# Performance work log

Measured on AMD Instinct MI355X. Metric: run time of the kernel, lower is better.

Reference implementation:

```python
import jax, jax.numpy as jnp
import numpy as np

B, T, D = 16, 2048, 256
QK = 64


def setup_inputs() -> dict:
    key = jax.random.key(0)
    ks = jax.random.split(key, 9)
    x = jax.random.normal(ks[0], (B, T, D), dtype=jnp.float32)
    sl = jax.random.uniform(ks[1], (B, T), dtype=jnp.float32)
    mask = jax.random.randint(ks[2], (B, T), 0, 2, dtype=jnp.int32)
    s = 1.0 / np.sqrt(D).astype(np.float32)
    Wq = jax.random.normal(ks[3], (QK, D), dtype=jnp.float32) * s
    bq = jnp.zeros((QK,), dtype=jnp.float32)
    Wk = jax.random.normal(ks[4], (QK, D), dtype=jnp.float32) * s
    bk = jnp.zeros((QK,), dtype=jnp.float32)
    Wv = jax.random.normal(ks[5], (D, D), dtype=jnp.float32) * s
    bv = jnp.zeros((D,), dtype=jnp.float32)
    return {"x": x, "sl": sl, "mask": mask, "Wq": Wq, "bq": bq,
            "Wk": Wk, "bk": bk, "Wv": Wv, "bv": bv}


def reference(x, sl, mask, Wq, bq, Wk, bk, Wv, bv):
    # x: [B,T,D], sl: [B,T] soft labels, mask: [B,T] valid positions
    sl = jnp.clip(sl, 0.0, 1.0)
    q = jnp.einsum('btd,ed->bte', x, Wq) + bq          # [B,T,QK]
    k = jnp.einsum('btd,ed->bte', x, Wk) + bk          # [B,T,QK]
    v = jnp.einsum('btd,ed->bte', x, Wv) + bv          # [B,T,D]
    scale = jnp.float32(1.0 / np.sqrt(QK))
    score = jnp.einsum('bte,bse->bts', q, k) * scale   # [B,T,T]
    # emotion scaling by (1 + sl_j^2) per key position j
    score = score * (1.0 + sl[:, None, :] ** 2)
    score = jnp.where(mask[:, None, :] == 0, jnp.float32(-1e9), score)
    prob = jax.nn.softmax(score, axis=-1)              # [B,T,T]
    out = jnp.einsum('bts,bsd->btd', prob, v)          # [B,T,D]
    return out.mean(axis=1)                            # [B,D]
```

## Files before the change

### kernel.cpp

```cpp
#include <hip/hip_runtime.h>
#include <hip/hip_bf16.h>
#include <stdint.h>

#define B_ 16
#define T_ 2048
#define D_ 256
#define QK_ 64
#define LOG2E 1.44269504088896340736f

typedef _Float16 f16;
typedef _Float16 f16x2 __attribute__((ext_vector_type(2)));
typedef __fp16 fp16x2 __attribute__((ext_vector_type(2)));
typedef _Float16 f16x8 __attribute__((ext_vector_type(8)));
typedef float f32x16 __attribute__((ext_vector_type(16)));

__device__ __forceinline__ void gload_lds16(const void* g, void* l) {
    __builtin_amdgcn_global_load_lds(
        (const __attribute__((address_space(1))) uint32_t*)g,
        (__attribute__((address_space(3))) uint32_t*)l, 16, 0, 0);
}

__device__ __forceinline__ float fexp2(float x) {
#if __has_builtin(__builtin_amdgcn_exp2f)
    return __builtin_amdgcn_exp2f(x);
#else
    return exp2f(x);
#endif
}
__device__ __forceinline__ float flog2(float x) {
#if __has_builtin(__builtin_amdgcn_logf)
    return __builtin_amdgcn_logf(x);
#else
    return log2f(x);
#endif
}
__device__ __forceinline__ f16x2 cvt2(float a, float b) {
#if __has_builtin(__builtin_amdgcn_cvt_pkrtz)
    fp16x2 r = __builtin_amdgcn_cvt_pkrtz(a, b);
    return __builtin_bit_cast(f16x2, r);
#else
    f16x2 r; r[0] = (f16)a; r[1] = (f16)b; return r;
#endif
}
__device__ __forceinline__ f16x8 cvt8(const float* p) {
    union { f16x2 h2[4]; f16x8 h8; } u;
    const float4 a0 = *(const float4*)p;
    const float4 a1 = *(const float4*)(p + 4);
    u.h2[0] = cvt2(a0.x, a0.y); u.h2[1] = cvt2(a0.z, a0.w);
    u.h2[2] = cvt2(a1.x, a1.y); u.h2[3] = cvt2(a1.z, a1.w);
    return u.h8;
}

__global__ __launch_bounds__(256) void proj_mfma(
    const float* __restrict__ x, const float* __restrict__ sl,
    const float* __restrict__ Wq, const float* __restrict__ Wk,
    const float* __restrict__ bq, const float* __restrict__ bk,
    f16* __restrict__ qh, f16* __restrict__ k2h,
    f16* __restrict__ qf, f16* __restrict__ kf)
{
    __shared__ __align__(16) f16 xs[32 * D_];
    __shared__ float ksc[32];
    const int b = blockIdx.y, tile = blockIdx.x, t0 = tile * 32;
    const int tid = threadIdx.x;
    const int wv = tid >> 6, l = tid & 63, lo = l & 31, hi = l >> 5;

    #pragma unroll
    for (int i = 0; i < 4; ++i) {
        const int f = i * 256 + tid;
        const int r = f >> 5, j = f & 31;
        const f16x8 h = cvt8(x + (size_t)(b * T_ + t0 + r) * D_ + j * 8);
        *(f16x8*)(xs + r * D_ + ((j ^ r) << 3)) = h;
    }
    if (tid < 32) {
        float s = sl[(size_t)b * T_ + t0 + tid];
        s = fminf(fmaxf(s, 0.f), 1.f);
        ksc[tid] = 0.125f * (1.f + s * s) * LOG2E;
    }
    __syncthreads();

    const int c0 = wv * 32;
    const int e = c0 + lo;
    const float* wrow = ((e < 64) ? (Wq + (size_t)e * D_)
                                  : (Wk + (size_t)(e - 64) * D_)) + hi * 8;

    f32x16 acc;
    #pragma unroll
    for (int i = 0; i < 16; ++i) acc[i] = 0.f;

    #pragma unroll
    for (int ks = 0; ks < 16; ++ks) {
        const f16x8 a  = *(const f16x8*)(xs + lo * D_ + ((((ks << 1) + hi) ^ lo) << 3));
        const f16x8 bf = cvt8(wrow + ks * 16);
        acc = __builtin_amdgcn_mfma_f32_32x32x16_f16(a, bf, acc, 0, 0, 0);
    }

    const float bias = (e < 64) ? bq[e] : bk[e - 64];
    __syncthreads();
    f16* hout = xs;
    #pragma unroll
    for (int i = 0; i < 16; ++i) {
        const int row = (i & 3) + 8 * (i >> 2) + 4 * hi;
        float v = acc[i] + bias;
        if (e >= 64) v *= ksc[row];
        hout[row * 128 + e] = (f16)v;
    }
    __syncthreads();
    #pragma unroll
    for (int i = 0; i < 2; ++i) {
        const int f = i * 256 + tid;
        const int rr = f >> 4, j = f & 15;
        const f16x8 v = *(const f16x8*)(hout + rr * 128 + j * 8);
        if (j < 8) *(f16x8*)(qh  + (size_t)(b * T_ + t0 + rr) * QK_ + j * 8) = v;
        else       *(f16x8*)(k2h + (size_t)(b * T_ + t0 + rr) * QK_ + (j - 8) * 8) = v;
    }
    {
        const int kc2 = tid >> 6, hi2 = (tid >> 5) & 1, lo2 = tid & 31;
        const f16* srcq = hout + lo2 * 128 + kc2 * 16 + hi2 * 8;
        const size_t tb = ((size_t)b * 64 + tile) * 2048 + tid * 8;
        *(f16x8*)(qf + tb) = *(const f16x8*)srcq;
        *(f16x8*)(kf + tb) = *(const f16x8*)(srcq + 64);
    }
}

__global__ __launch_bounds__(256) void z_part(
    const f16* __restrict__ qf, const f16* __restrict__ k2h,
    const int* __restrict__ mask, float* __restrict__ zpart)
{
    __shared__ __align__(16) f16 kt[128 * QK_];
    const int b = blockIdx.y;
    const int tIdx = blockIdx.x & 15, t0 = tIdx * 128;
    const int ck = blockIdx.x >> 4,  sbase = ck * 128;
    const int tid = threadIdx.x;
    const int wv = tid >> 6, l = tid & 63, lo = l & 31, hi = l >> 5;

    {
        const char* src = (const char*)(k2h + (size_t)(b * T_ + sbase) * QK_);
        #pragma unroll
        for (int i = 0; i < 4; ++i) {
            const int o = wv * 4096 + i * 1024 + l * 16;
            const int r = o >> 7, jc = (o >> 4) & 7;
            gload_lds16(src + r * 128 + ((jc ^ (r & 7)) << 4),
                        (char*)kt + wv * 4096 + i * 1024);
        }
    }

    const f16* abase = qf + ((size_t)b * 64 + tIdx * 4 + wv) * 2048 + l * 8;
    f16x8 a[4];
    #pragma unroll
    for (int kc = 0; kc < 4; ++kc) a[kc] = *(const f16x8*)(abase + kc * 512);

    float zp[16];
    #pragma unroll
    for (int i = 0; i < 16; ++i) zp[i] = 0.f;

    __syncthreads();

    #pragma unroll
    for (int cg = 0; cg < 4; ++cg) {
        const int srow = cg * 32 + lo;
        const float mb = mask[b * T_ + sbase + srow] ? 0.f : -1e9f;
        f32x16 c;
        #pragma unroll
        for (int i = 0; i < 16; ++i) c[i] = mb;
        #pragma unroll
        for (int kc = 0; kc < 4; ++kc) {
            const int jcc = (kc * 2 + hi) ^ (srow & 7);
            const f16x8 bf = *(const f16x8*)((const char*)kt + srow * 128 + (jcc << 4));
            c = __builtin_amdgcn_mfma_f32_32x32x16_f16(a[kc], bf, c, 0, 0, 0);
        }
        #pragma unroll
        for (int i = 0; i < 16; ++i) zp[i] += fexp2(c[i]);
    }

    __syncthreads();
    float* red = (float*)kt;
    #pragma unroll
    for (int i = 0; i < 16; ++i) {
        const int row = wv * 32 + (i & 3) + 8 * (i >> 2) + 4 * hi;
        const int col = (lo & 3) | ((((lo >> 2) ^ row) & 7) << 2);
        red[row * 32 + col] = zp[i];
    }
    __syncthreads();
    if (tid < 128) {
        float s = 0.f;
        #pragma unroll
        for (int c = 0; c < 8; ++c) {
            const float4 v = *(const float4*)(red + tid * 32 + (((c ^ tid) & 7) << 2));
            s += v.x + v.y + v.z + v.w;
        }
        zpart[(size_t)(b * 16 + ck) * T_ + t0 + tid] = s;
    }
}

__global__ __launch_bounds__(256) void w_part(
    const f16* __restrict__ kf, const f16* __restrict__ qh,
    const float* __restrict__ zpart, float* __restrict__ wpart)
{
    __shared__ __align__(16) f16 qt[128 * QK_];
    __shared__ float lz_s[128];
    const int b = blockIdx.y;
    const int sIdx = blockIdx.x & 15, s0b = sIdx * 128;
    const int tc = blockIdx.x >> 4,  tbase = tc * 128;
    const int tid = threadIdx.x;
    const int wv = tid >> 6, l = tid & 63, lo = l & 31, hi = l >> 5;

    {
        const char* src = (const char*)(qh + (size_t)(b * T_ + tbase) * QK_);
        #pragma unroll
        for (int i = 0; i < 4; ++i) {
            const int o = wv * 4096 + i * 1024 + l * 16;
            const int r = o >> 7, jc = (o >> 4) & 7;
            gload_lds16(src + r * 128 + ((jc ^ (r & 7)) << 4),
                        (char*)qt + wv * 4096 + i * 1024);
        }
    }
    if (tid < 128) {
        const float* zb = zpart + (size_t)(b * 16) * T_ + tbase + tid;
        float z = 0.f;
        #pragma unroll
        for (int ckk = 0; ckk < 16; ++ckk) z += zb[(size_t)ckk * T_];
        lz_s[tid] = -flog2(z);
    }

    const f16* abase = kf + ((size_t)b * 64 + sIdx * 4 + wv) * 2048 + l * 8;
    f16x8 a[4];
    #pragma unroll
    for (int kc = 0; kc < 4; ++kc) a[kc] = *(const f16x8*)(abase + kc * 512);

    float wp[16];
    #pragma unroll
    for (int i = 0; i < 16; ++i) wp[i] = 0.f;

    __syncthreads();

    #pragma unroll
    for (int cg = 0; cg < 4; ++cg) {
        const int trow = cg * 32 + lo;
        const float bias = lz_s[trow];
        f32x16 c;
        #pragma unroll
        for (int i = 0; i < 16; ++i) c[i] = bias;
        #pragma unroll
        for (int kc = 0; kc < 4; ++kc) {
            const int jcc = (kc * 2 + hi) ^ (trow & 7);
            const f16x8 bf = *(const f16x8*)((const char*)qt + trow * 128 + (jcc << 4));
            c = __builtin_amdgcn_mfma_f32_32x32x16_f16(a[kc], bf, c, 0, 0, 0);
        }
        #pragma unroll
        for (int i = 0; i < 16; ++i) wp[i] += fexp2(c[i]);
    }

    __syncthreads();
    float* red = (float*)qt;
    #pragma unroll
    for (int i = 0; i < 16; ++i) {
        const int row = wv * 32 + (i & 3) + 8 * (i >> 2) + 4 * hi;
        const int col = (lo & 3) | ((((lo >> 2) ^ row) & 7) << 2);
        red[row * 32 + col] = wp[i];
    }
    __syncthreads();
    if (tid < 128) {
        float s = 0.f;
        #pragma unroll
        for (int c = 0; c < 8; ++c) {
            const float4 v = *(const float4*)(red + tid * 32 + (((c ^ tid) & 7) << 2));
            s += v.x + v.y + v.z + v.w;
        }
        wpart[(size_t)(b * 16 + tc) * T_ + s0b + tid] = s;
    }
}

__global__ __launch_bounds__(256) void y_fused(
    const float* __restrict__ x, const float* __restrict__ wpart,
    const int* __restrict__ mask, float* __restrict__ ypart,
    float* __restrict__ swp)
{
    __shared__ float wloc[32];
    const int b  = blockIdx.y;
    const int ch = blockIdx.x;
    const int tid = threadIdx.x;

    if (tid < 32) {
        const int s = ch * 32 + tid;
        const float* wb = wpart + (size_t)(b * 16) * T_ + s;
        float v = 0.f;
        #pragma unroll
        for (int ckk = 0; ckk < 16; ++ckk) v += wb[(size_t)ckk * T_];
        v *= mask[b * T_ + s] ? (1.f / (float)T_) : 0.f;
        wloc[tid] = v;
        float sv = v;
        #pragma unroll
        for (int off = 1; off <= 16; off <<= 1) sv += __shfl_xor(sv, off);
        if (tid == 0) swp[b * 64 + ch] = sv;
    }
    __syncthreads();

    const int d = tid;
    const float* xb = x + ((size_t)b * T_ + ch * 32) * D_;
    float acc = 0.f;
    #pragma unroll 8
    for (int s = 0; s < 32; ++s) acc += wloc[s] * xb[(size_t)s * D_ + d];
    ypart[((size_t)b * 64 + ch) * D_ + d] = acc;
}

__global__ __launch_bounds__(256) void outkernel(
    const float* __restrict__ ypart, const float* __restrict__ swp,
    const float* __restrict__ Wv, const float* __restrict__ bv,
    float* __restrict__ out)
{
    __shared__ __align__(16) float ys[D_];
    __shared__ float sw0;
    const int b   = blockIdx.x;
    const int tid = threadIdx.x;

    float yv = 0.f;
    #pragma unroll
    for (int ch = 0; ch < 64; ++ch) yv += ypart[((size_t)b * 64 + ch) * D_ + tid];
    ys[tid] = yv;

    float s = (tid < 64) ? swp[b * 64 + tid] : 0.f;
    #pragma unroll
    for (int off = 1; off <= 32; off <<= 1) s += __shfl_xor(s, off);
    if (tid == 0) sw0 = s;
    __syncthreads();

    const float sw = sw0;
    const float4* wv4 = (const float4*)(Wv + (size_t)tid * D_);
    const float4* ys4 = (const float4*)ys;
    float o = 0.f;
    for (int i = 0; i < D_ / 4; ++i) {
        const float4 a = wv4[i];
        const float4 y = ys4[i];
        o += a.x * y.x + a.y * y.y + a.z * y.z + a.w * y.w;
    }
    out[(size_t)b * D_ + tid] = o + bv[tid] * sw;
}

extern "C" void kernel_launch(void* const* d_in, const int* in_sizes, int n_in,
                              void* d_out, int out_size, void* d_ws, size_t ws_size,
                              hipStream_t stream)
{
    const float* x    = (const float*)d_in[0];
    const float* sl   = (const float*)d_in[1];
    const int*   mask = (const int*)d_in[2];
    const float* Wq   = (const float*)d_in[3];
    const float* bq   = (const float*)d_in[4];
    const float* Wk   = (const float*)d_in[5];
    const float* bk   = (const float*)d_in[6];
    const float* Wv   = (const float*)d_in[7];
    const float* bv   = (const float*)d_in[8];
    float* out = (float*)d_out;

    f16*   qh    = (f16*)d_ws;
    f16*   k2h   = qh  + (size_t)B_ * T_ * QK_;
    f16*   qf    = k2h + (size_t)B_ * T_ * QK_;
    f16*   kf    = qf  + (size_t)B_ * T_ * QK_;
    float* zpart = (float*)(kf + (size_t)B_ * T_ * QK_);
    float* wpart = zpart + (size_t)B_ * 16 * T_;
    float* swp   = wpart + (size_t)B_ * 16 * T_;
    float* yp    = swp + B_ * 64;

    proj_mfma<<<dim3(T_ / 32, B_), 256, 0, stream>>>(x, sl, Wq, Wk, bq, bk, qh, k2h, qf, kf);
    z_part   <<<dim3(256, B_), 256, 0, stream>>>(qf, k2h, mask, zpart);
    w_part   <<<dim3(256, B_), 256, 0, stream>>>(kf, qh, zpart, wpart);
    y_fused  <<<dim3(64, B_), 256, 0, stream>>>(x, wpart, mask, yp, swp);
    outkernel<<<dim3(B_), 256, 0, stream>>>(yp, swp, Wv, bv, out);
}
```

Measured before the change: 82.60 us.

## Read fragment-layout K/Q directly from global and halve key-chunk split

The score kernels stop staging row-major K/Q tiles into LDS via global_load_lds and instead read MFMA-fragment-ordered q/k buffers directly from global memory into registers. This removes the qh/k2h outputs from the projection kernel. Each block now covers 256 key or query positions instead of 128, so there are half as many partial chunks to reduce and half as many blocks. In exchange, operand loads go through global/L2 without LDS reuse across waves, and grids are smaller, which lowers parallelism.

```diff
diff --git a/kernel.cpp b/kernel.cpp
--- a/kernel.cpp
+++ b/kernel.cpp
@@ -1,5 +1,4 @@
 #include <hip/hip_runtime.h>
-#include <hip/hip_bf16.h>
 #include <stdint.h>
 
 #define B_ 16
@@ -7,18 +6,13 @@
 #define D_ 256
 #define QK_ 64
 #define LOG2E 1.44269504088896340736f
+#define NCH 8
 
 typedef _Float16 f16;
 typedef _Float16 f16x2 __attribute__((ext_vector_type(2)));
 typedef __fp16 fp16x2 __attribute__((ext_vector_type(2)));
 typedef _Float16 f16x8 __attribute__((ext_vector_type(8)));
 typedef float f32x16 __attribute__((ext_vector_type(16)));
-
-__device__ __forceinline__ void gload_lds16(const void* g, void* l) {
-    __builtin_amdgcn_global_load_lds(
-        (const __attribute__((address_space(1))) uint32_t*)g,
-        (__attribute__((address_space(3))) uint32_t*)l, 16, 0, 0);
-}
 
 __device__ __forceinline__ float fexp2(float x) {
 #if __has_builtin(__builtin_amdgcn_exp2f)
@@ -51,18 +45,18 @@
     return u.h8;
 }
 
-__global__ __launch_bounds__(256) void proj_mfma(
+
+__global__ __launch_bounds__(256, 4) void kP(
     const float* __restrict__ x, const float* __restrict__ sl,
-    const float* __restrict__ Wq, const float* __restrict__ Wk,
-    const float* __restrict__ bq, const float* __restrict__ bk,
-    f16* __restrict__ qh, f16* __restrict__ k2h,
+    const float* __restrict__ Wq, const float* __restrict__ bq,
+    const float* __restrict__ Wk, const float* __restrict__ bk,
     f16* __restrict__ qf, f16* __restrict__ kf)
 {
     __shared__ __align__(16) f16 xs[32 * D_];
     __shared__ float ksc[32];
+    const int tid = threadIdx.x;
+    const int wv = tid >> 6, l = tid & 63, lo = l & 31, hi = l >> 5;
     const int b = blockIdx.y, tile = blockIdx.x, t0 = tile * 32;
-    const int tid = threadIdx.x;
-    const int wv = tid >> 6, l = tid & 63, lo = l & 31, hi = l >> 5;
 
     #pragma unroll
     for (int i = 0; i < 4; ++i) {
@@ -78,22 +72,18 @@
     }
     __syncthreads();
 
-    const int c0 = wv * 32;
-    const int e = c0 + lo;
+    const int e = wv * 32 + lo;
     const float* wrow = ((e < 64) ? (Wq + (size_t)e * D_)
                                   : (Wk + (size_t)(e - 64) * D_)) + hi * 8;
-
     f32x16 acc;
     #pragma unroll
     for (int i = 0; i < 16; ++i) acc[i] = 0.f;
-
     #pragma unroll
     for (int ks = 0; ks < 16; ++ks) {
         const f16x8 a  = *(const f16x8*)(xs + lo * D_ + ((((ks << 1) + hi) ^ lo) << 3));
         const f16x8 bf = cvt8(wrow + ks * 16);
         acc = __builtin_amdgcn_mfma_f32_32x32x16_f16(a, bf, acc, 0, 0, 0);
     }
-
     const float bias = (e < 64) ? bq[e] : bk[e - 64];
     __syncthreads();
     f16* hout = xs;
@@ -105,44 +95,22 @@
         hout[row * 128 + e] = (f16)v;
     }
     __syncthreads();
-    #pragma unroll
-    for (int i = 0; i < 2; ++i) {
-        const int f = i * 256 + tid;
-        const int rr = f >> 4, j = f & 15;
-        const f16x8 v = *(const f16x8*)(hout + rr * 128 + j * 8);
-        if (j < 8) *(f16x8*)(qh  + (size_t)(b * T_ + t0 + rr) * QK_ + j * 8) = v;
-        else       *(f16x8*)(k2h + (size_t)(b * T_ + t0 + rr) * QK_ + (j - 8) * 8) = v;
-    }
-    {
-        const int kc2 = tid >> 6, hi2 = (tid >> 5) & 1, lo2 = tid & 31;
-        const f16* srcq = hout + lo2 * 128 + kc2 * 16 + hi2 * 8;
-        const size_t tb = ((size_t)b * 64 + tile) * 2048 + tid * 8;
-        *(f16x8*)(qf + tb) = *(const f16x8*)srcq;
-        *(f16x8*)(kf + tb) = *(const f16x8*)(srcq + 64);
-    }
-}
-
-__global__ __launch_bounds__(256) void z_part(
-    const f16* __restrict__ qf, const f16* __restrict__ k2h,
+    const int kc2 = tid >> 6, hi2 = (tid >> 5) & 1, lo2 = tid & 31;
+    const f16* srcq = hout + lo2 * 128 + kc2 * 16 + hi2 * 8;
+    const size_t tb = ((size_t)b * 64 + tile) * 2048 + tid * 8;
+    *(f16x8*)(qf + tb) = *(const f16x8*)srcq;
+    *(f16x8*)(kf + tb) = *(const f16x8*)(srcq + 64);
+}
+
+__global__ __launch_bounds__(256, 4) void kZ(
+    const f16* __restrict__ qf, const f16* __restrict__ kf,
     const int* __restrict__ mask, float* __restrict__ zpart)
 {
-    __shared__ __align__(16) f16 kt[128 * QK_];
+    __shared__ __align__(16) float red[128 * 32];
+    const int tid = threadIdx.x;
+    const int wv = tid >> 6, l = tid & 63, lo = l & 31, hi = l >> 5;
     const int b = blockIdx.y;
-    const int tIdx = blockIdx.x & 15, t0 = tIdx * 128;
-    const int ck = blockIdx.x >> 4,  sbase = ck * 128;
-    const int tid = threadIdx.x;
-    const int wv = tid >> 6, l = tid & 63, lo = l & 31, hi = l >> 5;
-
-    {
-        const char* src = (const char*)(k2h + (size_t)(b * T_ + sbase) * QK_);
-        #pragma unroll
-        for (int i = 0; i < 4; ++i) {
-            const int o = wv * 4096 + i * 1024 + l * 16;
-            const int r = o >> 7, jc = (o >> 4) & 7;
-            gload_lds16(src + r * 128 + ((jc ^ (r & 7)) << 4),
-                        (char*)kt + wv * 4096 + i * 1024);
-        }
-    }
+    const int tIdx = blockIdx.x >> 3, ckg = blockIdx.x & 7;
 
     const f16* abase = qf + ((size_t)b * 64 + tIdx * 4 + wv) * 2048 + l * 8;
     f16x8 a[4];
@@ -153,27 +121,22 @@
     #pragma unroll
     for (int i = 0; i < 16; ++i) zp[i] = 0.f;
 
-    __syncthreads();
-
-    #pragma unroll
-    for (int cg = 0; cg < 4; ++cg) {
-        const int srow = cg * 32 + lo;
-        const float mb = mask[b * T_ + sbase + srow] ? 0.f : -1e9f;
+    #pragma unroll
+    for (int g = 0; g < 8; ++g) {
+        const int stile = ckg * 8 + g;
+        const float mb = mask[b * T_ + stile * 32 + lo] ? 0.f : -1e9f;
+        const f16* bbase = kf + ((size_t)b * 64 + stile) * 2048 + l * 8;
         f32x16 c;
         #pragma unroll
         for (int i = 0; i < 16; ++i) c[i] = mb;
         #pragma unroll
         for (int kc = 0; kc < 4; ++kc) {
-            const int jcc = (kc * 2 + hi) ^ (srow & 7);
-            const f16x8 bf = *(const f16x8*)((const char*)kt + srow * 128 + (jcc << 4));
+            const f16x8 bf = *(const f16x8*)(bbase + kc * 512);
             c = __builtin_amdgcn_mfma_f32_32x32x16_f16(a[kc], bf, c, 0, 0, 0);
         }
         #pragma unroll
         for (int i = 0; i < 16; ++i) zp[i] += fexp2(c[i]);
     }
-
-    __syncthreads();
-    float* red = (float*)kt;
     #pragma unroll
     for (int i = 0; i < 16; ++i) {
         const int row = wv * 32 + (i & 3) + 8 * (i >> 2) + 4 * hi;
@@ -188,40 +151,28 @@
             const float4 v = *(const float4*)(red + tid * 32 + (((c ^ tid) & 7) << 2));
             s += v.x + v.y + v.z + v.w;
         }
-        zpart[(size_t)(b * 16 + ck) * T_ + t0 + tid] = s;
-    }
-}
-
-__global__ __launch_bounds__(256) void w_part(
-    const f16* __restrict__ kf, const f16* __restrict__ qh,
+        zpart[(size_t)(b * NCH + ckg) * T_ + tIdx * 128 + tid] = s;
+    }
+}
+
+__global__ __launch_bounds__(256, 4) void kW(
+    const f16* __restrict__ qf, const f16* __restrict__ kf,
     const float* __restrict__ zpart, float* __restrict__ wpart)
 {
-    __shared__ __align__(16) f16 qt[128 * QK_];
-    __shared__ float lz_s[128];
+    __shared__ __align__(16) float red[128 * 32];
+    __shared__ float lz_s[256];
+    const int tid = threadIdx.x;
+    const int wv = tid >> 6, l = tid & 63, lo = l & 31, hi = l >> 5;
     const int b = blockIdx.y;
-    const int sIdx = blockIdx.x & 15, s0b = sIdx * 128;
-    const int tc = blockIdx.x >> 4,  tbase = tc * 128;
-    const int tid = threadIdx.x;
-    const int wv = tid >> 6, l = tid & 63, lo = l & 31, hi = l >> 5;
+    const int sIdx = blockIdx.x >> 3, tcg = blockIdx.x & 7;
 
     {
-        const char* src = (const char*)(qh + (size_t)(b * T_ + tbase) * QK_);
-        #pragma unroll
-        for (int i = 0; i < 4; ++i) {
-            const int o = wv * 4096 + i * 1024 + l * 16;
-            const int r = o >> 7, jc = (o >> 4) & 7;
-            gload_lds16(src + r * 128 + ((jc ^ (r & 7)) << 4),
-                        (char*)qt + wv * 4096 + i * 1024);
-        }
-    }
-    if (tid < 128) {
-        const float* zb = zpart + (size_t)(b * 16) * T_ + tbase + tid;
+        const float* zb = zpart + (size_t)(b * NCH) * T_ + tcg * 256 + tid;
         float z = 0.f;
         #pragma unroll
-        for (int ckk = 0; ckk < 16; ++ckk) z += zb[(size_t)ckk * T_];
+        for (int ck = 0; ck < NCH; ++ck) z += zb[(size_t)ck * T_];
         lz_s[tid] = -flog2(z);
     }
-
     const f16* abase = kf + ((size_t)b * 64 + sIdx * 4 + wv) * 2048 + l * 8;
     f16x8 a[4];
     #pragma unroll
@@ -230,28 +181,24 @@
     float wp[16];
     #pragma unroll
     for (int i = 0; i < 16; ++i) wp[i] = 0.f;
-
-    __syncthreads();
-
-    #pragma unroll
-    for (int cg = 0; cg < 4; ++cg) {
-        const int trow = cg * 32 + lo;
-        const float bias = lz_s[trow];
+    __syncthreads();
+
+    #pragma unroll
+    for (int g = 0; g < 8; ++g) {
+        const int qtile = tcg * 8 + g;
+        const float bias = lz_s[g * 32 + lo];
+        const f16* bbase = qf + ((size_t)b * 64 + qtile) * 2048 + l * 8;
         f32x16 c;
         #pragma unroll
         for (int i = 0; i < 16; ++i) c[i] = bias;
         #pragma unroll
         for (int kc = 0; kc < 4; ++kc) {
-            const int jcc = (kc * 2 + hi) ^ (trow & 7);
-            const f16x8 bf = *(const f16x8*)((const char*)qt + trow * 128 + (jcc << 4));
+            const f16x8 bf = *(const f16x8*)(bbase + kc * 512);
             c = __builtin_amdgcn_mfma_f32_32x32x16_f16(a[kc], bf, c, 0, 0, 0);
         }
         #pragma unroll
         for (int i = 0; i < 16; ++i) wp[i] += fexp2(c[i]);
     }
-
-    __syncthreads();
-    float* red = (float*)qt;
     #pragma unroll
     for (int i = 0; i < 16; ++i) {
         const int row = wv * 32 + (i & 3) + 8 * (i >> 2) + 4 * hi;
@@ -266,11 +213,11 @@
             const float4 v = *(const float4*)(red + tid * 32 + (((c ^ tid) & 7) << 2));
             s += v.x + v.y + v.z + v.w;
         }
-        wpart[(size_t)(b * 16 + tc) * T_ + s0b + tid] = s;
-    }
-}
-
-__global__ __launch_bounds__(256) void y_fused(
+        wpart[(size_t)(b * NCH + tcg) * T_ + sIdx * 128 + tid] = s;
+    }
+}
+
+__global__ __launch_bounds__(256, 4) void kY(
     const float* __restrict__ x, const float* __restrict__ wpart,
     const int* __restrict__ mask, float* __restrict__ ypart,
     float* __restrict__ swp)
@@ -282,10 +229,10 @@
 
     if (tid < 32) {
         const int s = ch * 32 + tid;
-        const float* wb = wpart + (size_t)(b * 16) * T_ + s;
+        const float* wb = wpart + (size_t)(b * NCH) * T_ + s;
         float v = 0.f;
         #pragma unroll
-        for (int ckk = 0; ckk < 16; ++ckk) v += wb[(size_t)ckk * T_];
+        for (int ck = 0; ck < NCH; ++ck) v += wb[(size_t)ck * T_];
         v *= mask[b * T_ + s] ? (1.f / (float)T_) : 0.f;
         wloc[tid] = v;
         float sv = v;
@@ -294,16 +241,14 @@
         if (tid == 0) swp[b * 64 + ch] = sv;
     }
     __syncthreads();
-
-    const int d = tid;
     const float* xb = x + ((size_t)b * T_ + ch * 32) * D_;
     float acc = 0.f;
     #pragma unroll 8
-    for (int s = 0; s < 32; ++s) acc += wloc[s] * xb[(size_t)s * D_ + d];
-    ypart[((size_t)b * 64 + ch) * D_ + d] = acc;
-}
-
-__global__ __launch_bounds__(256) void outkernel(
+    for (int s = 0; s < 32; ++s) acc += wloc[s] * xb[(size_t)s * D_ + tid];
+    ypart[((size_t)b * 64 + ch) * D_ + tid] = acc;
+}
+
+__global__ __launch_bounds__(256, 4) void kOUT(
     const float* __restrict__ ypart, const float* __restrict__ swp,
     const float* __restrict__ Wv, const float* __restrict__ bv,
     float* __restrict__ out)
@@ -317,17 +262,16 @@
     #pragma unroll
     for (int ch = 0; ch < 64; ++ch) yv += ypart[((size_t)b * 64 + ch) * D_ + tid];
     ys[tid] = yv;
-
     float s = (tid < 64) ? swp[b * 64 + tid] : 0.f;
     #pragma unroll
     for (int off = 1; off <= 32; off <<= 1) s += __shfl_xor(s, off);
     if (tid == 0) sw0 = s;
     __syncthreads();
-
     const float sw = sw0;
     const float4* wv4 = (const float4*)(Wv + (size_t)tid * D_);
     const float4* ys4 = (const float4*)ys;
     float o = 0.f;
+    #pragma unroll
     for (int i = 0; i < D_ / 4; ++i) {
         const float4 a = wv4[i];
         const float4 y = ys4[i];
@@ -351,18 +295,16 @@
     const float* bv   = (const float*)d_in[8];
     float* out = (float*)d_out;
 
-    f16*   qh    = (f16*)d_ws;
-    f16*   k2h   = qh  + (size_t)B_ * T_ * QK_;
-    f16*   qf    = k2h + (size_t)B_ * T_ * QK_;
-    f16*   kf    = qf  + (size_t)B_ * T_ * QK_;
+    f16*   qf    = (f16*)d_ws;
+    f16*   kf    = qf + (size_t)B_ * T_ * QK_;
     float* zpart = (float*)(kf + (size_t)B_ * T_ * QK_);
-    float* wpart = zpart + (size_t)B_ * 16 * T_;
-    float* swp   = wpart + (size_t)B_ * 16 * T_;
+    float* wpart = zpart + (size_t)B_ * NCH * T_;
+    float* swp   = wpart + (size_t)B_ * NCH * T_;
     float* yp    = swp + B_ * 64;
 
-    proj_mfma<<<dim3(T_ / 32, B_), 256, 0, stream>>>(x, sl, Wq, Wk, bq, bk, qh, k2h, qf, kf);
-    z_part   <<<dim3(256, B_), 256, 0, stream>>>(qf, k2h, mask, zpart);
-    w_part   <<<dim3(256, B_), 256, 0, stream>>>(kf, qh, zpart, wpart);
-    y_fused  <<<dim3(64, B_), 256, 0, stream>>>(x, wpart, mask, yp, swp);
-    outkernel<<<dim3(B_), 256, 0, stream>>>(yp, swp, Wv, bv, out);
-}
+    kP  <<<dim3(64, B_), 256, 0, stream>>>(x, sl, Wq, bq, Wk, bk, qf, kf);
+    kZ  <<<dim3(128, B_), 256, 0, stream>>>(qf, kf, mask, zpart);
+    kW  <<<dim3(128, B_), 256, 0, stream>>>(qf, kf, zpart, wpart);
+    kY  <<<dim3(64, B_), 256, 0, stream>>>(x, wpart, mask, yp, swp);
+    kOUT<<<dim3(B_), 256, 0, stream>>>(yp, swp, Wv, bv, out);
+}
```

Result: slower. 93.47 us (+13.2%).
